# Performance work log

Measured on AMD Instinct MI355X. Metric: run time of the kernel, lower is better.

Reference implementation:

```python
import jax, jax.numpy as jnp
import numpy as np

B, S, DIM = 4, 3968, 512
H, HD = 8, 64
CHUNK, NPM, MEM = 496, 32, 1024  # MEM == NPM + 2*CHUNK (required by module's EMA update broadcast)


def _lin(k, din, dout):
    kw, kb = jax.random.split(k)
    w = jax.random.normal(kw, (din, dout), jnp.float32) / np.sqrt(din)
    b = jax.random.normal(kb, (dout,), jnp.float32) * 0.01
    return w, b


def setup_inputs() -> dict:
    key = jax.random.key(0)
    ks = jax.random.split(key, 12)
    inp = {}
    inp["x"] = jax.random.normal(ks[0], (B, S, DIM), jnp.float32)
    inp["persistent_memory"] = jax.random.normal(ks[1], (NPM, DIM), jnp.float32)
    # outer query projection
    inp["Wq_out"], inp["bq_out"] = _lin(ks[2], DIM, DIM)
    # NeuralMemory projections
    inp["mk_w"], inp["mk_b"] = _lin(ks[3], DIM, DIM)
    inp["mv_w"], inp["mv_b"] = _lin(ks[4], DIM, DIM)
    inp["mq_w"], inp["mq_b"] = _lin(ks[5], DIM, DIM)
    # TitanAttention (standard MHA: q/k/v to H*HD, out proj back to DIM)
    inp["aq_w"], inp["aq_b"] = _lin(ks[6], DIM, H * HD)
    inp["ak_w"], inp["ak_b"] = _lin(ks[7], DIM, H * HD)
    inp["av_w"], inp["av_b"] = _lin(ks[8], DIM, H * HD)
    inp["ao_w"], inp["ao_b"] = _lin(ks[9], H * HD, DIM)
    return inp


def reference(x, persistent_memory, Wq_out, bq_out,
              mk_w, mk_b, mv_w, mv_b, mq_w, mq_b,
              aq_w, aq_b, ak_w, ak_b, av_w, av_b, ao_w, ao_b):
    Bn, Sn, D = x.shape
    nch = Sn // CHUNK
    inv_sqrt_d = 1.0 / np.sqrt(D).astype(np.float32)
    inv_sqrt_hd = 1.0 / np.sqrt(HD).astype(np.float32)

    def retrieve(mem, q):
        # mem: [B, MEM, D], q: [B, L, D]
        qp = q @ mq_w + mq_b
        k = mem @ mk_w + mk_b
        v = mem @ mv_w + mv_b
        sc = jnp.einsum('bqd,bmd->bqm', qp, k) * inv_sqrt_d
        a = jax.nn.softmax(sc, axis=-1)
        return jnp.einsum('bqm,bmd->bqd', a, v)

    def mha(t):
        # t: [B, L, D] -> [B, L, D]; dropout inactive (eval)
        Bm, L, _ = t.shape
        q = (t @ aq_w + aq_b).reshape(Bm, L, H, HD)
        k = (t @ ak_w + ak_b).reshape(Bm, L, H, HD)
        v = (t @ av_w + av_b).reshape(Bm, L, H, HD)
        sc = jnp.einsum('bqhd,bkhd->bhqk', q, k) * inv_sqrt_hd
        a = jax.nn.softmax(sc, axis=-1)
        o = jnp.einsum('bhqk,bkhd->bqhd', a, v).reshape(Bm, L, H * HD)
        return o @ ao_w + ao_b

    pm = jnp.broadcast_to(persistent_memory[None], (Bn, NPM, D))
    chunks = x.reshape(Bn, nch, CHUNK, D).transpose(1, 0, 2, 3)  # [nch, B, C, D]
    mem0 = jnp.zeros((Bn, MEM, D), x.dtype)

    def step(mem, chunk):
        query = chunk @ Wq_out + bq_out
        hist = retrieve(mem, query)                              # [B, C, D]
        combined = jnp.concatenate([pm, hist, chunk], axis=1)    # [B, MEM, D]
        attended = mha(combined)
        mem2 = 0.9 * mem + 0.1 * attended                        # EMA update
        mout = retrieve(mem2, attended)
        out = (attended * mout)[:, -CHUNK:]                      # keep last chunk slice
        return mem2, out

    _, outs = jax.lax.scan(step, mem0, chunks)                   # outs: [nch, B, C, D]
    return outs.transpose(1, 0, 2, 3).reshape(Bn, Sn, D)
```

## Files before the change

### kernel.cpp

```cpp
#include <hip/hip_runtime.h>
#include <hip/hip_fp16.h>


typedef __attribute__((ext_vector_type(8))) short short8;
typedef __attribute__((ext_vector_type(4))) float f32x4;

static __device__ __forceinline__ unsigned short f32_bf16(float f) {
  unsigned int u = __float_as_uint(f);
  u += 0x7FFFu + ((u >> 16) & 1u);
  return (unsigned short)(u >> 16);
}
static __device__ __forceinline__ unsigned pk(float lo, float hi) {
  return (unsigned)f32_bf16(lo) | ((unsigned)f32_bf16(hi) << 16);
}

template<int BM, int BN, int ATY, int BTY, int CTY, bool GUARD, bool BIAS>
__global__ __launch_bounds__(256) void gemm2(
    const void* __restrict__ Ap, long long Asb, long long Ash, int Ars,
    const void* __restrict__ Bp, long long Bsb, long long Bsh, int Brs,
    void* __restrict__ Cp, long long Csb, long long Csh, int Crs,
    void* __restrict__ Cp2, int csplit, void* __restrict__ Cp3,
    const float* __restrict__ bias, float scale, int M, int Kdim, int Hh)
{
  constexpr int LDP = 72;
  constexpr int WN = (BN >= 128) ? 2 : (BM >= 128 ? 1 : 2);
  constexpr int WM = 4 / WN;
  constexpr int MI = BM / (WM * 16);
  constexpr int NI = BN / (WN * 16);
  constexpr int AP = BM / 32;
  constexpr int BP = BN / 32;

  __shared__ unsigned short As[2][BM][LDP];
  __shared__ unsigned short Bs[2][BN][LDP];

  const int tid  = threadIdx.x;
  const int lane = tid & 63;
  const int w    = tid >> 6;
  const int wm   = w / WN, wn = w % WN;
  const int z    = blockIdx.z;
  const int zb   = z / Hh, zh = z - zb * Hh;
  const int m0   = blockIdx.x * BM;
  const int n0   = blockIdx.y * BN;
  const int lrow = lane & 15;
  const int lkB  = (lane >> 4) * 8;
  const int srow = tid >> 3;
  const int scol = (tid & 7) * 8;

  const float*          Af  = (const float*)Ap          + zb * Asb + zh * Ash;
  const unsigned short* Ahp = (const unsigned short*)Ap + zb * Asb + zh * Ash;
  const float*          Bf  = (const float*)Bp          + zb * Bsb + zh * Bsh;
  const unsigned short* Bhp = (const unsigned short*)Bp + zb * Bsb + zh * Bsh;

  float4 afl[AP][2]; uint4 ahl[AP];
  float4 bfl[BP][2]; uint4 bhl[BP];

  auto loadT = [&](int k0) {
    #pragma unroll
    for (int p = 0; p < AP; ++p) {
      const int row = srow + p * 32;
      const bool ok = !GUARD || (m0 + row) < M;
      if constexpr (ATY == 0) {
        if (ok) {
          const float* s = Af + (long long)(m0 + row) * Ars + k0 + scol;
          afl[p][0] = *(const float4*)s;
          afl[p][1] = *(const float4*)(s + 4);
        } else {
          afl[p][0] = make_float4(0.f,0.f,0.f,0.f);
          afl[p][1] = make_float4(0.f,0.f,0.f,0.f);
        }
      } else {
        ahl[p] = ok ? *(const uint4*)(Ahp + (long long)(m0 + row) * Ars + k0 + scol)
                    : make_uint4(0u,0u,0u,0u);
      }
    }
    #pragma unroll
    for (int p = 0; p < BP; ++p) {
      const int row = srow + p * 32;
      if constexpr (BTY == 0) {
        const float* s = Bf + (long long)(n0 + row) * Brs + k0 + scol;
        bfl[p][0] = *(const float4*)s;
        bfl[p][1] = *(const float4*)(s + 4);
      } else {
        bhl[p] = *(const uint4*)(Bhp + (long long)(n0 + row) * Brs + k0 + scol);
      }
    }
  };
  auto writeT = [&](int buf) {
    #pragma unroll
    for (int p = 0; p < AP; ++p) {
      const int row = srow + p * 32;
      uint4 u;
      if constexpr (ATY == 0) {
        u.x = pk(afl[p][0].x, afl[p][0].y); u.y = pk(afl[p][0].z, afl[p][0].w);
        u.z = pk(afl[p][1].x, afl[p][1].y); u.w = pk(afl[p][1].z, afl[p][1].w);
      } else u = ahl[p];
      *(uint4*)(&As[buf][row][scol]) = u;
    }
    #pragma unroll
    for (int p = 0; p < BP; ++p) {
      const int row = srow + p * 32;
      uint4 u;
      if constexpr (BTY == 0) {
        u.x = pk(bfl[p][0].x, bfl[p][0].y); u.y = pk(bfl[p][0].z, bfl[p][0].w);
        u.z = pk(bfl[p][1].x, bfl[p][1].y); u.w = pk(bfl[p][1].z, bfl[p][1].w);
      } else u = bhl[p];
      *(uint4*)(&Bs[buf][row][scol]) = u;
    }
  };

  f32x4 acc[MI][NI] = {};

  loadT(0);
  writeT(0);
  __syncthreads();

  const int NT = Kdim >> 6;
  int cur = 0;
  for (int t = 0; t < NT; ++t) {
    const bool more = (t + 1) < NT;
    if (more) loadT((t + 1) << 6);

    short8 a8[MI][2], b8[NI][2];
    #pragma unroll
    for (int mi = 0; mi < MI; ++mi) {
      const unsigned short* r = &As[cur][wm * (MI * 16) + mi * 16 + lrow][lkB];
      a8[mi][0] = *(const short8*)r;
      a8[mi][1] = *(const short8*)(r + 32);
    }
    #pragma unroll
    for (int ni = 0; ni < NI; ++ni) {
      const unsigned short* r = &Bs[cur][wn * (NI * 16) + ni * 16 + lrow][lkB];
      b8[ni][0] = *(const short8*)r;
      b8[ni][1] = *(const short8*)(r + 32);
    }
    #pragma unroll
    for (int kk = 0; kk < 2; ++kk)
      #pragma unroll
      for (int mi = 0; mi < MI; ++mi)
        #pragma unroll
        for (int ni = 0; ni < NI; ++ni)
          acc[mi][ni] = __builtin_amdgcn_mfma_f32_16x16x32_bf16(a8[mi][kk], b8[ni][kk], acc[mi][ni], 0, 0, 0);

    if (more) writeT(cur ^ 1);
    __syncthreads();
    cur ^= 1;
  }

  float*          Cf  = (float*)Cp          + zb * Csb + zh * Csh;
  unsigned short* Chn = (unsigned short*)Cp + zb * Csb + zh * Csh;
  unsigned short* Ch2 = (unsigned short*)Cp2;
  unsigned short* Kb3 = (unsigned short*)Cp3;
  const bool trside = (CTY == 4 || CTY == 5) ? (n0 >= csplit) : false;

  #pragma unroll
  for (int ni = 0; ni < NI; ++ni) {
    const int col = n0 + wn * (NI * 16) + ni * 16 + lrow;
    const float bv = BIAS ? bias[col] : 0.0f;
    #pragma unroll
    for (int mi = 0; mi < MI; ++mi) {
      const int rbase = m0 + wm * (MI * 16) + mi * 16 + ((lane >> 4) << 2);
      if constexpr (CTY == 5) {
        ushort4 vt;
        #pragma unroll
        for (int r = 0; r < 4; ++r) {
          const int row = rbase + r;
          const float proj = acc[mi][ni][r] * scale + bv;
          const long long midx = (long long)row * Crs + col;
          const float v = 0.9f * Cf[midx] + 0.1f * proj;
          Cf[midx] = v;
          if (!trside) Kb3[(long long)row * 512 + col] = f32_bf16(v);
          else ((unsigned short*)&vt)[r] = f32_bf16(v);
        }
        if (trside)
          *(ushort4*)(&Ch2[(long long)(rbase >> 10) * 524288
                           + (long long)(col - csplit) * 1024 + (rbase & 1023)]) = vt;
      } else if constexpr (CTY == 6) {
        const float* ATTp = (const float*)Cp2;
        float* Of = (float*)Cp;
        #pragma unroll
        for (int r = 0; r < 4; ++r) {
          const int row = rbase + r;
          if (row < M) {
            const float v = acc[mi][ni][r] * scale;
            const float a = ATTp[((long long)zb * 496 + row) * 512 + col];
            Of[((long long)zb * 3968 + (long long)csplit * 496 + row) * 512 + col] = v * a;
          }
        }
      } else if (trside) {
        ushort4 v;
        v.x = f32_bf16(acc[mi][ni][0] * scale + bv);
        v.y = f32_bf16(acc[mi][ni][1] * scale + bv);
        v.z = f32_bf16(acc[mi][ni][2] * scale + bv);
        v.w = f32_bf16(acc[mi][ni][3] * scale + bv);
        *(ushort4*)(&Ch2[(long long)(rbase >> 10) * 524288
                         + (long long)(col - csplit) * 1024 + (rbase & 1023)]) = v;
      } else {
        #pragma unroll
        for (int r = 0; r < 4; ++r) {
          const int row = rbase + r;
          if (!GUARD || row < M) {
            const float v = acc[mi][ni][r] * scale + bv;
            if constexpr (CTY == 0)      Cf [(long long)row * Crs + col] = v;
            else                         Chn[(long long)row * Crs + col] = f32_bf16(v);
          }
        }
      }
    }
  }
}

__global__ __launch_bounds__(256) void flash_mha(
    const unsigned short* __restrict__ QK, const unsigned short* __restrict__ Vt,
    unsigned short* __restrict__ OH)
{
  __shared__ unsigned short Ks[128][72];
  __shared__ unsigned short Vs[64][136];
  __shared__ unsigned short Ps[64][136];

  const int tid = threadIdx.x, lane = tid & 63, w = tid >> 6;
  const int f = blockIdx.x;
  const int xcd = f & 7, j = f >> 3;
  const int bh = xcd + 8 * (j >> 4);
  const int qt = j & 15;
  const int b = bh >> 3, h = bh & 7;
  const int q0 = qt * 64;
  const unsigned short* Qp = QK + (long long)b * 1048576 + h * 64;
  const unsigned short* Kp = Qp + 512;
  const unsigned short* Vp = Vt + (long long)b * 524288 + (long long)(h * 64) * 1024;
  unsigned short* Op = OH + (long long)b * 524288 + h * 64;

  const int lr = lane & 15, g = lane >> 4, lk = g * 8;
  const int wq = w * 16;

  short8 qb[2];
  qb[0] = *(const short8*)(Qp + (long long)(q0 + wq + lr) * 1024 + lk);
  qb[1] = *(const short8*)(Qp + (long long)(q0 + wq + lr) * 1024 + 32 + lk);

  const int krow = tid >> 1, kcol = (tid & 1) * 32;
  const int vrow = tid >> 2, vcol = (tid & 3) * 32;

  uint4 kl[4], vl[4];
  auto loadKV = [&](int kt) {
    #pragma unroll
    for (int jj = 0; jj < 4; ++jj)
      kl[jj] = *(const uint4*)(Kp + (long long)(kt * 128 + krow) * 1024 + kcol + jj * 8);
    #pragma unroll
    for (int jj = 0; jj < 4; ++jj)
      vl[jj] = *(const uint4*)(Vp + (long long)vrow * 1024 + kt * 128 + vcol + jj * 8);
  };
  auto writeKV = [&]() {
    #pragma unroll
    for (int jj = 0; jj < 4; ++jj) *(uint4*)(&Ks[krow][kcol + jj * 8]) = kl[jj];
    #pragma unroll
    for (int jj = 0; jj < 4; ++jj) *(uint4*)(&Vs[vrow][vcol + jj * 8]) = vl[jj];
  };

  loadKV(0); writeKV();
  __syncthreads();

  f32x4 acc[4] = {};
  float m = -1e30f, l = 0.f;

  for (int kt = 0; kt < 8; ++kt) {
    const bool more = kt < 7;
    if (more) loadKV(kt + 1);

    f32x4 s[8] = {};
    #pragma unroll
    for (int ks = 0; ks < 2; ++ks)
      #pragma unroll
      for (int ni = 0; ni < 8; ++ni) {
        const short8 ka = *(const short8*)(&Ks[ni * 16 + lr][ks * 32 + lk]);
        s[ni] = __builtin_amdgcn_mfma_f32_16x16x32_bf16(ka, qb[ks], s[ni], 0, 0, 0);
      }

    float rm = -1e30f;
    #pragma unroll
    for (int ni = 0; ni < 8; ++ni)
      #pragma unroll
      for (int r = 0; r < 4; ++r) { s[ni][r] *= 0.125f; rm = fmaxf(rm, s[ni][r]); }
    rm = fmaxf(rm, __shfl_xor(rm, 16));
    rm = fmaxf(rm, __shfl_xor(rm, 32));

    const float mn = fmaxf(m, rm);
    const float al = __expf(m - mn);
    m = mn;
    float ls = 0.f;
    #pragma unroll
    for (int ni = 0; ni < 8; ++ni)
      #pragma unroll
      for (int r = 0; r < 4; ++r) { s[ni][r] = __expf(s[ni][r] - m); ls += s[ni][r]; }
    ls += __shfl_xor(ls, 16);
    ls += __shfl_xor(ls, 32);
    l = l * al + ls;
    #pragma unroll
    for (int nd = 0; nd < 4; ++nd)
      #pragma unroll
      for (int r = 0; r < 4; ++r) acc[nd][r] *= al;

    #pragma unroll
    for (int ni = 0; ni < 8; ++ni)
      #pragma unroll
      for (int r = 0; r < 4; ++r)
        Ps[wq + lr][ni * 16 + (g << 2) + r] = f32_bf16(s[ni][r]);

    #pragma unroll
    for (int ks2 = 0; ks2 < 4; ++ks2) {
      const short8 pb = *(const short8*)(&Ps[wq + lr][ks2 * 32 + lk]);
      #pragma unroll
      for (int nd = 0; nd < 4; ++nd) {
        const short8 va = *(const short8*)(&Vs[nd * 16 + lr][ks2 * 32 + lk]);
        acc[nd] = __builtin_amdgcn_mfma_f32_16x16x32_bf16(va, pb, acc[nd], 0, 0, 0);
      }
    }

    __syncthreads();
    if (more) { writeKV(); __syncthreads(); }
  }

  unsigned short (*Os)[72] = (unsigned short (*)[72])&Ks[0][0];
  const float inv = 1.0f / l;
  #pragma unroll
  for (int nd = 0; nd < 4; ++nd)
    #pragma unroll
    for (int r = 0; r < 4; ++r)
      Os[wq + lr][nd * 16 + (g << 2) + r] = f32_bf16(acc[nd][r] * inv);
  __syncthreads();
  const int orow = tid >> 2, ocol = (tid & 3) * 16;
  const uint4 u0 = *(const uint4*)(&Os[orow][ocol]);
  const uint4 u1 = *(const uint4*)(&Os[orow][ocol + 8]);
  *(uint4*)(Op + (long long)(q0 + orow) * 512 + ocol) = u0;
  *(uint4*)(Op + (long long)(q0 + orow) * 512 + ocol + 8) = u1;
}

struct TP7 { const float* s[7]; unsigned short* d[7]; };
__global__ __launch_bounds__(256) void transpose7(TP7 tp)
{
  __shared__ float tile[32][33];
  const float* in = tp.s[blockIdx.z];
  unsigned short* out = tp.d[blockIdx.z];
  const int c0 = blockIdx.x * 32, r0 = blockIdx.y * 32;
  const int xx = threadIdx.x & 31, ys = threadIdx.x >> 5;
  #pragma unroll
  for (int yy = ys; yy < 32; yy += 8)
    tile[yy][xx] = in[(long long)(r0 + yy) * 512 + c0 + xx];
  __syncthreads();
  #pragma unroll
  for (int yy = ys; yy < 32; yy += 8)
    out[(long long)(c0 + yy) * 512 + r0 + xx] = f32_bf16(tile[xx][yy]);
}

__global__ __launch_bounds__(256) void softmax_rows_bf(
    const float* __restrict__ buf, unsigned short* __restrict__ obuf,
    int rowsPerZ, long long zStride)
{
  const int gr   = blockIdx.x * 4 + (threadIdx.x >> 6);
  const int lane = threadIdx.x & 63;
  const int z = gr / rowsPerZ;
  const int i = gr - z * rowsPerZ;
  const float* pf = buf + (long long)z * zStride + (long long)i * 1024 + lane * 16;
  float v[16];
  #pragma unroll
  for (int j = 0; j < 4; ++j) {
    const float4 f = ((const float4*)pf)[j];
    v[4*j+0] = f.x; v[4*j+1] = f.y; v[4*j+2] = f.z; v[4*j+3] = f.w;
  }
  float mx = v[0];
  #pragma unroll
  for (int j = 1; j < 16; ++j) mx = fmaxf(mx, v[j]);
  #pragma unroll
  for (int d = 32; d; d >>= 1) mx = fmaxf(mx, __shfl_xor(mx, d));
  float s = 0.0f;
  #pragma unroll
  for (int j = 0; j < 16; ++j) { v[j] = __expf(v[j] - mx); s += v[j]; }
  #pragma unroll
  for (int d = 32; d; d >>= 1) s += __shfl_xor(s, d);
  const float inv = 1.0f / s;
  unsigned short* ph = obuf + (long long)z * zStride + (long long)i * 1024 + lane * 16;
  unsigned uu[8];
  #pragma unroll
  for (int j = 0; j < 8; ++j) uu[j] = pk(v[2*j] * inv, v[2*j+1] * inv);
  ((uint4*)ph)[0] = make_uint4(uu[0], uu[1], uu[2], uu[3]);
  ((uint4*)ph)[1] = make_uint4(uu[4], uu[5], uu[6], uu[7]);
}

__global__ __launch_bounds__(256) void copy_pm8(const float* __restrict__ pm, unsigned short* __restrict__ comb8)
{
  const int ci = blockIdx.y;
  const int idx = blockIdx.x * 256 + threadIdx.x;
  const int b = idx >> 11, e = idx & 2047;
  const int row = e >> 6, d8 = (e & 63) * 8;
  const float* s = pm + row * 512 + d8;
  const float4 f0 = *(const float4*)s;
  const float4 f1 = *(const float4*)(s + 4);
  uint4 u; u.x = pk(f0.x, f0.y); u.y = pk(f0.z, f0.w); u.z = pk(f1.x, f1.y); u.w = pk(f1.z, f1.w);
  *(uint4*)(comb8 + (long long)ci * 2097152 + (long long)b * 524288 + row * 512 + d8) = u;
}

__global__ __launch_bounds__(256) void copy_chunk8(const float* __restrict__ x, unsigned short* __restrict__ comb8)
{
  const int ci = blockIdx.y;
  const int idx = blockIdx.x * 256 + threadIdx.x;
  const int b = idx / 31744, e = idx % 31744;
  const int row = e >> 6, d8 = (e & 63) * 8;
  const float* s = x + ((long long)b * 3968 + ci * 496 + row) * 512 + d8;
  const float4 f0 = *(const float4*)s;
  const float4 f1 = *(const float4*)(s + 4);
  uint4 u; u.x = pk(f0.x, f0.y); u.y = pk(f0.z, f0.w); u.z = pk(f1.x, f1.y); u.w = pk(f1.z, f1.w);
  *(uint4*)(comb8 + (long long)ci * 2097152 + (long long)b * 524288 + (528 + row) * 512 + d8) = u;
}

__global__ __launch_bounds__(256) void init_kv(const float* __restrict__ mkb, const float* __restrict__ mvb,
                                               float* __restrict__ master, unsigned short* __restrict__ Kb)
{
  const int idx = blockIdx.x * 256 + threadIdx.x;
  const int c4 = (idx & 255) * 4;
  const long long row = idx >> 8;
  const float4 v = *(const float4*)((c4 < 512) ? (mkb + c4) : (mvb + c4 - 512));
  *(float4*)(master + row * 1024 + c4) = v;
  if (c4 < 512) {
    ushort4 h; h.x = f32_bf16(v.x); h.y = f32_bf16(v.y); h.z = f32_bf16(v.z); h.w = f32_bf16(v.w);
    *(ushort4*)(Kb + row * 512 + c4) = h;
  }
}

__global__ __launch_bounds__(256) void init_vt(const float* __restrict__ mvb, unsigned short* __restrict__ VT)
{
  const int idx = blockIdx.x * 256 + threadIdx.x;
  const int k8 = (idx & 127) * 8;
  const int d  = (idx >> 7) & 511;
  const int b  = idx >> 16;
  const unsigned short hv = f32_bf16(mvb[d]);
  const ushort4 h4 = make_ushort4(hv, hv, hv, hv);
  unsigned short* dst = VT + (long long)b * 524288 + (long long)d * 1024 + k8;
  *(ushort4*)dst = h4; *(ushort4*)(dst + 4) = h4;
}

__global__ __launch_bounds__(256) void fuse_bias(const float* __restrict__ bq, const float* __restrict__ mq,
                                                 const float* __restrict__ mqb, float* __restrict__ bqm)
{
  const int c = blockIdx.x * 256 + threadIdx.x;
  float s = mqb[c];
  for (int j = 0; j < 512; ++j) s += bq[j] * mq[j * 512 + c];
  bqm[c] = s;
}

__global__ __launch_bounds__(256) void fuse_bias2(const float* __restrict__ aob,
                                                  const float* __restrict__ mkw, const float* __restrict__ mkb,
                                                  const float* __restrict__ mvw, const float* __restrict__ mvb,
                                                  float* __restrict__ baokv)
{
  const int c = blockIdx.x * 256 + threadIdx.x;
  const float* w  = (c < 512) ? mkw : mvw;
  const float* bb = (c < 512) ? mkb : mvb;
  const int cc = c & 511;
  float s = bb[cc];
  for (int j = 0; j < 512; ++j) s += aob[j] * w[j * 512 + cc];
  baokv[c] = s;
}

extern "C" void kernel_launch(void* const* d_in, const int* in_sizes, int n_in,
                              void* d_out, int out_size, void* d_ws, size_t ws_size,
                              hipStream_t stream)
{
  (void)in_sizes; (void)n_in; (void)out_size; (void)ws_size;
  const float* x   = (const float*)d_in[0];
  const float* pm  = (const float*)d_in[1];
  const float* Wq  = (const float*)d_in[2];
  const float* bq  = (const float*)d_in[3];
  const float* mkw = (const float*)d_in[4];
  const float* mkb = (const float*)d_in[5];
  const float* mvw = (const float*)d_in[6];
  const float* mvb = (const float*)d_in[7];
  const float* mqw = (const float*)d_in[8];
  const float* mqb = (const float*)d_in[9];
  const float* aqw = (const float*)d_in[10];
  const float* aqb = (const float*)d_in[11];
  const float* akw = (const float*)d_in[12];
  const float* akb = (const float*)d_in[13];
  const float* avw = (const float*)d_in[14];
  const float* avb = (const float*)d_in[15];
  const float* aow = (const float*)d_in[16];
  const float* aob = (const float*)d_in[17];
  float* out = (float*)d_out;

  char* wsp = (char*)d_ws;
  size_t off = 0;
  auto alloc = [&](size_t b) -> void* { void* p = wsp + off; off += (b + 255) & ~(size_t)255; return p; };

  unsigned short* WTmq  = (unsigned short*)alloc(524288);
  unsigned short* WKV   = (unsigned short*)alloc(1048576);
  unsigned short* WQKV  = (unsigned short*)alloc(1572864);
  unsigned short* WTao  = (unsigned short*)alloc(524288);
  unsigned short* Wqm   = (unsigned short*)alloc(524288);
  unsigned short* WaoKV = (unsigned short*)alloc(1048576);
  unsigned short* Waomq = (unsigned short*)alloc(524288);
  float* bqkv  = (float*)alloc(6144);
  float* bqm   = (float*)alloc(2048);
  float* baokv = (float*)alloc(4096);
  float* baomq = (float*)alloc(2048);
  float*          master = (float*)alloc(16777216);
  unsigned short* Kb   = (unsigned short*)alloc(4194304);
  unsigned short* VT   = (unsigned short*)alloc(4194304);
  unsigned short* VTm  = (unsigned short*)alloc(4194304);
  unsigned short* QP1  = (unsigned short*)alloc(16252928);
  unsigned short* QP   = (unsigned short*)alloc(2031616);
  unsigned short* comb8= (unsigned short*)alloc(33554432);
  unsigned short* QKb  = (unsigned short*)alloc(8388608);
  unsigned short* OH   = (unsigned short*)alloc(4194304);
  float*          ATT  = (float*)alloc(4063232);
  float*          SC   = (float*)alloc(8126464);
  unsigned short* SCb  = (unsigned short*)alloc(4063232);

  const long long XBS = 2031616, BS = 524288, QBS = 253952;
  const long long SCB = 507904;
  const float sr = 0.044194173824159216f;

  TP7 tp;
  tp.s[0] = mqw; tp.d[0] = WTmq;
  tp.s[1] = mkw; tp.d[1] = WKV;
  tp.s[2] = mvw; tp.d[2] = WKV + 262144;
  tp.s[3] = aqw; tp.d[3] = WQKV;
  tp.s[4] = akw; tp.d[4] = WQKV + 262144;
  tp.s[5] = avw; tp.d[5] = WQKV + 524288;
  tp.s[6] = aow; tp.d[6] = WTao;
  transpose7<<<dim3(16,16,7),256,0,stream>>>(tp);
  gemm2<64,64,1,0,2,false,false><<<dim3(8,8,1),256,0,stream>>>(
    WTmq, 0, 0, 512, Wq, 0, 0, 512, Wqm, 0, 0, 512,
    nullptr, 0, nullptr, nullptr, 1.0f, 512, 512, 1);
  gemm2<64,64,1,0,2,false,false><<<dim3(16,8,1),256,0,stream>>>(
    WKV, 0, 0, 512, aow, 0, 0, 512, WaoKV, 0, 0, 512,
    nullptr, 0, nullptr, nullptr, 1.0f, 1024, 512, 1);
  gemm2<64,64,1,0,2,false,false><<<dim3(8,8,1),256,0,stream>>>(
    WTmq, 0, 0, 512, aow, 0, 0, 512, Waomq, 0, 0, 512,
    nullptr, 0, nullptr, nullptr, 1.0f, 512, 512, 1);
  fuse_bias<<<2,256,0,stream>>>(bq, mqw, mqb, bqm);
  fuse_bias<<<2,256,0,stream>>>(aob, mqw, mqb, baomq);
  fuse_bias2<<<4,256,0,stream>>>(aob, mkw, mkb, mvw, mvb, baokv);
  gemm2<128,64,0,1,2,false,true><<<dim3(124,8,1),256,0,stream>>>(
    x, 0, 0, 512, Wqm, 0, 0, 512,
    QP1, 0, 0, 512, nullptr, 0, nullptr, bqm, 1.0f, 15872, 512, 1);
  hipMemcpyAsync(bqkv,       aqb, 2048, hipMemcpyDeviceToDevice, stream);
  hipMemcpyAsync(bqkv + 512, akb, 2048, hipMemcpyDeviceToDevice, stream);
  hipMemcpyAsync(bqkv +1024, avb, 2048, hipMemcpyDeviceToDevice, stream);
  init_kv<<<4096,256,0,stream>>>(mkb, mvb, master, Kb);
  init_vt<<<1024,256,0,stream>>>(mvb, VT);
  copy_pm8<<<dim3(32,8),256,0,stream>>>(pm, comb8);
  copy_chunk8<<<dim3(496,8),256,0,stream>>>(x, comb8);

  for (int ci = 0; ci < 8; ++ci) {
    unsigned short* comb = comb8 + (long long)ci * 2097152;

    gemm2<64,64,1,1,0,true,false><<<dim3(8,16,4),256,0,stream>>>(
      QP1 + (long long)ci * 253952, XBS, 0, 512, Kb, BS, 0, 512,
      SC, SCB, 0, 1024, nullptr, 0, nullptr, nullptr, sr, 496, 512, 1);
    softmax_rows_bf<<<496,256,0,stream>>>(SC, SCb, 496, SCB);
    gemm2<64,64,1,1,2,true,false><<<dim3(8,8,4),256,0,stream>>>(
      SCb, SCB, 0, 1024, VT, BS, 0, 1024,
      comb + 32 * 512, BS, 0, 512, nullptr, 0, nullptr, nullptr, 1.0f, 496, 1024, 1);

    gemm2<128,64,1,1,4,false,true><<<dim3(32,24,1),256,0,stream>>>(
      comb, 0, 0, 512, WQKV, 0, 0, 512,
      QKb, 0, 0, 1024, VTm, 1024, nullptr, bqkv, 1.0f, 4096, 512, 1);
    flash_mha<<<512,256,0,stream>>>(QKb, VTm, OH);

    gemm2<128,64,1,1,5,false,true><<<dim3(32,16,1),256,0,stream>>>(
      OH, 0, 0, 512, WaoKV, 0, 0, 512,
      master, 0, 0, 1024, VT, 512, Kb, baokv, 1.0f, 4096, 512, 1);
    gemm2<64,64,1,1,2,true,true><<<dim3(8,8,4),256,0,stream>>>(
      OH + 528 * 512, BS, 0, 512, Waomq, 0, 0, 512,
      QP, QBS, 0, 512, nullptr, 0, nullptr, baomq, 1.0f, 496, 512, 1);
    gemm2<64,64,1,1,0,true,true><<<dim3(8,8,4),256,0,stream>>>(
      OH + 528 * 512, BS, 0, 512, WTao, 0, 0, 512,
      ATT, QBS, 0, 512, nullptr, 0, nullptr, aob, 1.0f, 496, 512, 1);

    gemm2<64,64,1,1,0,true,false><<<dim3(8,16,4),256,0,stream>>>(
      QP, QBS, 0, 512, Kb, BS, 0, 512,
      SC, SCB, 0, 1024, nullptr, 0, nullptr, nullptr, sr, 496, 512, 1);
    softmax_rows_bf<<<496,256,0,stream>>>(SC, SCb, 496, SCB);
    gemm2<64,64,1,1,6,true,false><<<dim3(8,8,4),256,0,stream>>>(
      SCb, SCB, 0, 1024, VT, BS, 0, 1024,
      out, 0, 0, 512, ATT, ci, nullptr, nullptr, 1.0f, 496, 1024, 1);
  }
}
```

Before: 1.346 ms.

## Split flash attention over KV halves with combine kernel; merge two output GEMMs

The flash MHA kernel now splits the 1024-key range into two halves per query tile, doubling the block count to 1024. It writes unnormalised fp32 partial outputs plus row max and sum, and a new combine kernel merges them with softmax rescaling into the bf16 head output. Separately, the two GEMMs that map OH to QP (bf16) and ATT (fp32) are fused into one GEMM over a concatenated weight and bias, using a new epilogue that routes columns to each destination. This adds fp32 partial-buffer traffic and one extra launch per chunk in exchange for better occupancy and one fewer GEMM launch.

```diff
diff --git a/kernel.cpp b/kernel.cpp
--- a/kernel.cpp
+++ b/kernel.cpp
@@ -186,6 +186,19 @@
             Of[((long long)zb * 3968 + (long long)csplit * 496 + row) * 512 + col] = v * a;
           }
         }
+      } else if constexpr (CTY == 8) {
+        float* ATTo = (float*)Cp2;
+        #pragma unroll
+        for (int r = 0; r < 4; ++r) {
+          const int row = rbase + r;
+          if (row < M) {
+            const float v = acc[mi][ni][r] * scale + bv;
+            if (col < csplit)
+              Kb3[((long long)zb * 496 + row) * 512 + col] = f32_bf16(v);
+            else
+              ATTo[((long long)zb * 496 + row) * 512 + (col - csplit)] = v;
+          }
+        }
       } else if (trside) {
         ushort4 v;
         v.x = f32_bf16(acc[mi][ni][0] * scale + bv);
@@ -209,9 +222,9 @@
   }
 }
 
-__global__ __launch_bounds__(256) void flash_mha(
+__global__ __launch_bounds__(256) void flash_mha_ks(
     const unsigned short* __restrict__ QK, const unsigned short* __restrict__ Vt,
-    unsigned short* __restrict__ OH)
+    float* __restrict__ Opart, float* __restrict__ ML)
 {
   __shared__ unsigned short Ks[128][72];
   __shared__ unsigned short Vs[64][136];
@@ -220,14 +233,14 @@
   const int tid = threadIdx.x, lane = tid & 63, w = tid >> 6;
   const int f = blockIdx.x;
   const int xcd = f & 7, j = f >> 3;
-  const int bh = xcd + 8 * (j >> 4);
-  const int qt = j & 15;
+  const int bh = xcd + 8 * (j >> 5);
+  const int jj = j & 31;
+  const int qt = jj >> 1, part = jj & 1;
   const int b = bh >> 3, h = bh & 7;
-  const int q0 = qt * 64;
+  const int q0 = qt * 64, koff = part * 4;
   const unsigned short* Qp = QK + (long long)b * 1048576 + h * 64;
   const unsigned short* Kp = Qp + 512;
   const unsigned short* Vp = Vt + (long long)b * 524288 + (long long)(h * 64) * 1024;
-  unsigned short* Op = OH + (long long)b * 524288 + h * 64;
 
   const int lr = lane & 15, g = lane >> 4, lk = g * 8;
   const int wq = w * 16;
@@ -242,28 +255,28 @@
   uint4 kl[4], vl[4];
   auto loadKV = [&](int kt) {
     #pragma unroll
-    for (int jj = 0; jj < 4; ++jj)
-      kl[jj] = *(const uint4*)(Kp + (long long)(kt * 128 + krow) * 1024 + kcol + jj * 8);
-    #pragma unroll
-    for (int jj = 0; jj < 4; ++jj)
-      vl[jj] = *(const uint4*)(Vp + (long long)vrow * 1024 + kt * 128 + vcol + jj * 8);
+    for (int jx = 0; jx < 4; ++jx)
+      kl[jx] = *(const uint4*)(Kp + (long long)(kt * 128 + krow) * 1024 + kcol + jx * 8);
+    #pragma unroll
+    for (int jx = 0; jx < 4; ++jx)
+      vl[jx] = *(const uint4*)(Vp + (long long)vrow * 1024 + kt * 128 + vcol + jx * 8);
   };
   auto writeKV = [&]() {
     #pragma unroll
-    for (int jj = 0; jj < 4; ++jj) *(uint4*)(&Ks[krow][kcol + jj * 8]) = kl[jj];
-    #pragma unroll
-    for (int jj = 0; jj < 4; ++jj) *(uint4*)(&Vs[vrow][vcol + jj * 8]) = vl[jj];
+    for (int jx = 0; jx < 4; ++jx) *(uint4*)(&Ks[krow][kcol + jx * 8]) = kl[jx];
+    #pragma unroll
+    for (int jx = 0; jx < 4; ++jx) *(uint4*)(&Vs[vrow][vcol + jx * 8]) = vl[jx];
   };
 
-  loadKV(0); writeKV();
+  loadKV(koff); writeKV();
   __syncthreads();
 
   f32x4 acc[4] = {};
   float m = -1e30f, l = 0.f;
 
-  for (int kt = 0; kt < 8; ++kt) {
-    const bool more = kt < 7;
-    if (more) loadKV(kt + 1);
+  for (int it = 0; it < 4; ++it) {
+    const bool more = it < 3;
+    if (more) loadKV(koff + it + 1);
 
     f32x4 s[8] = {};
     #pragma unroll
@@ -314,23 +327,60 @@
       }
     }
 
-    __syncthreads();
-    if (more) { writeKV(); __syncthreads(); }
-  }
-
-  unsigned short (*Os)[72] = (unsigned short (*)[72])&Ks[0][0];
-  const float inv = 1.0f / l;
+    if (more) { __syncthreads(); writeKV(); __syncthreads(); }
+  }
+
+  const int pbq = (bh * 16 + qt) * 2 + part;
+  float* Ob = Opart + (long long)pbq * 4096;
   #pragma unroll
   for (int nd = 0; nd < 4; ++nd)
     #pragma unroll
     for (int r = 0; r < 4; ++r)
-      Os[wq + lr][nd * 16 + (g << 2) + r] = f32_bf16(acc[nd][r] * inv);
+      Ob[(16 * nd + 4 * g + r) * 64 + wq + lr] = acc[nd][r];
+  if (g == 0) {
+    ML[pbq * 128 + wq + lr] = m;
+    ML[pbq * 128 + 64 + wq + lr] = l;
+  }
+}
+
+__global__ __launch_bounds__(256) void combine_mha(
+    const float* __restrict__ Opart, const float* __restrict__ ML,
+    unsigned short* __restrict__ OH)
+{
+  __shared__ float Oc[64][65];
+  __shared__ float w1s[64], w2s[64], wis[64];
+  const int t = threadIdx.x;
+  const int bq = blockIdx.x;
+  const int bh = bq >> 4, qt = bq & 15, b = bh >> 3, h = bh & 7, q0 = qt * 64;
+  const float* O1 = Opart + (long long)(bq * 2 + 0) * 4096;
+  const float* O2 = Opart + (long long)(bq * 2 + 1) * 4096;
+  const float* ml1 = ML + (bq * 2 + 0) * 128;
+  const float* ml2 = ML + (bq * 2 + 1) * 128;
+  if (t < 64) {
+    const float m1 = ml1[t], l1 = ml1[64 + t], m2 = ml2[t], l2 = ml2[64 + t];
+    const float mm = fmaxf(m1, m2);
+    const float e1 = __expf(m1 - mm), e2 = __expf(m2 - mm);
+    w1s[t] = e1; w2s[t] = e2; wis[t] = 1.0f / (e1 * l1 + e2 * l2);
+  }
   __syncthreads();
-  const int orow = tid >> 2, ocol = (tid & 3) * 16;
-  const uint4 u0 = *(const uint4*)(&Os[orow][ocol]);
-  const uint4 u1 = *(const uint4*)(&Os[orow][ocol + 8]);
-  *(uint4*)(Op + (long long)(q0 + orow) * 512 + ocol) = u0;
-  *(uint4*)(Op + (long long)(q0 + orow) * 512 + ocol + 8) = u1;
+  {
+    const int d = t >> 2, qs = (t & 3) * 16;
+    #pragma unroll
+    for (int i = 0; i < 16; ++i) {
+      const int q = qs + i;
+      Oc[d][q] = (w1s[q] * O1[d * 64 + q] + w2s[q] * O2[d * 64 + q]) * wis[q];
+    }
+  }
+  __syncthreads();
+  {
+    const int q = t >> 2, ds = (t & 3) * 16;
+    unsigned short tmp[16];
+    #pragma unroll
+    for (int i = 0; i < 16; ++i) tmp[i] = f32_bf16(Oc[ds + i][q]);
+    unsigned short* dst = OH + (long long)b * 524288 + (long long)(q0 + q) * 512 + h * 64 + ds;
+    *(uint4*)dst = *(uint4*)&tmp[0];
+    *(uint4*)(dst + 8) = *(uint4*)&tmp[8];
+  }
 }
 
 struct TP7 { const float* s[7]; unsigned short* d[7]; };
@@ -491,14 +541,13 @@
   unsigned short* WTmq  = (unsigned short*)alloc(524288);
   unsigned short* WKV   = (unsigned short*)alloc(1048576);
   unsigned short* WQKV  = (unsigned short*)alloc(1572864);
-  unsigned short* WTao  = (unsigned short*)alloc(524288);
   unsigned short* Wqm   = (unsigned short*)alloc(524288);
   unsigned short* WaoKV = (unsigned short*)alloc(1048576);
-  unsigned short* Waomq = (unsigned short*)alloc(524288);
+  unsigned short* WQA   = (unsigned short*)alloc(1048576);
   float* bqkv  = (float*)alloc(6144);
   float* bqm   = (float*)alloc(2048);
   float* baokv = (float*)alloc(4096);
-  float* baomq = (float*)alloc(2048);
+  float* bqa   = (float*)alloc(4096);
   float*          master = (float*)alloc(16777216);
   unsigned short* Kb   = (unsigned short*)alloc(4194304);
   unsigned short* VT   = (unsigned short*)alloc(4194304);
@@ -511,6 +560,8 @@
   float*          ATT  = (float*)alloc(4063232);
   float*          SC   = (float*)alloc(8126464);
   unsigned short* SCb  = (unsigned short*)alloc(4063232);
+  float*          Opart= (float*)alloc(16777216);
+  float*          ML   = (float*)alloc(524288);
 
   const long long XBS = 2031616, BS = 524288, QBS = 253952;
   const long long SCB = 507904;
@@ -523,7 +574,7 @@
   tp.s[3] = aqw; tp.d[3] = WQKV;
   tp.s[4] = akw; tp.d[4] = WQKV + 262144;
   tp.s[5] = avw; tp.d[5] = WQKV + 524288;
-  tp.s[6] = aow; tp.d[6] = WTao;
+  tp.s[6] = aow; tp.d[6] = WQA + 262144;
   transpose7<<<dim3(16,16,7),256,0,stream>>>(tp);
   gemm2<64,64,1,0,2,false,false><<<dim3(8,8,1),256,0,stream>>>(
     WTmq, 0, 0, 512, Wq, 0, 0, 512, Wqm, 0, 0, 512,
@@ -532,11 +583,12 @@
     WKV, 0, 0, 512, aow, 0, 0, 512, WaoKV, 0, 0, 512,
     nullptr, 0, nullptr, nullptr, 1.0f, 1024, 512, 1);
   gemm2<64,64,1,0,2,false,false><<<dim3(8,8,1),256,0,stream>>>(
-    WTmq, 0, 0, 512, aow, 0, 0, 512, Waomq, 0, 0, 512,
+    WTmq, 0, 0, 512, aow, 0, 0, 512, WQA, 0, 0, 512,
     nullptr, 0, nullptr, nullptr, 1.0f, 512, 512, 1);
   fuse_bias<<<2,256,0,stream>>>(bq, mqw, mqb, bqm);
-  fuse_bias<<<2,256,0,stream>>>(aob, mqw, mqb, baomq);
+  fuse_bias<<<2,256,0,stream>>>(aob, mqw, mqb, bqa);
   fuse_bias2<<<4,256,0,stream>>>(aob, mkw, mkb, mvw, mvb, baokv);
+  hipMemcpyAsync(bqa + 512, aob, 2048, hipMemcpyDeviceToDevice, stream);
   gemm2<128,64,0,1,2,false,true><<<dim3(124,8,1),256,0,stream>>>(
     x, 0, 0, 512, Wqm, 0, 0, 512,
     QP1, 0, 0, 512, nullptr, 0, nullptr, bqm, 1.0f, 15872, 512, 1);
@@ -562,17 +614,15 @@
     gemm2<128,64,1,1,4,false,true><<<dim3(32,24,1),256,0,stream>>>(
       comb, 0, 0, 512, WQKV, 0, 0, 512,
       QKb, 0, 0, 1024, VTm, 1024, nullptr, bqkv, 1.0f, 4096, 512, 1);
-    flash_mha<<<512,256,0,stream>>>(QKb, VTm, OH);
+    flash_mha_ks<<<1024,256,0,stream>>>(QKb, VTm, Opart, ML);
+    combine_mha<<<512,256,0,stream>>>(Opart, ML, OH);
 
     gemm2<128,64,1,1,5,false,true><<<dim3(32,16,1),256,0,stream>>>(
       OH, 0, 0, 512, WaoKV, 0, 0, 512,
       master, 0, 0, 1024, VT, 512, Kb, baokv, 1.0f, 4096, 512, 1);
-    gemm2<64,64,1,1,2,true,true><<<dim3(8,8,4),256,0,stream>>>(
-      OH + 528 * 512, BS, 0, 512, Waomq, 0, 0, 512,
-      QP, QBS, 0, 512, nullptr, 0, nullptr, baomq, 1.0f, 496, 512, 1);
-    gemm2<64,64,1,1,0,true,true><<<dim3(8,8,4),256,0,stream>>>(
-      OH + 528 * 512, BS, 0, 512, WTao, 0, 0, 512,
-      ATT, QBS, 0, 512, nullptr, 0, nullptr, aob, 1.0f, 496, 512, 1);
+    gemm2<64,64,1,1,8,true,true><<<dim3(8,16,4),256,0,stream>>>(
+      OH + 528 * 512, BS, 0, 512, WQA, 0, 0, 512,
+      nullptr, 0, 0, 512, ATT, 512, QP, bqa, 1.0f, 496, 512, 1);
 
     gemm2<64,64,1,1,0,true,false><<<dim3(8,16,4),256,0,stream>>>(
       QP, QBS, 0, 512, Kb, BS, 0, 512,
```

Result: no change. 1.320 ms (-1.9%).
